# Kernel optimization log

Measured on AMD Instinct MI355X. Metric: run time of the kernel, lower is better.

The kernel has to match this reference:

```python
import jax, jax.numpy as jnp
import numpy as np

EPS = 1e-5

def rmsnorm(x, w):
    var = jnp.mean(x * x, axis=-1, keepdims=True)
    return x * jax.lax.rsqrt(var + EPS) * w


def setup_inputs() -> dict:
    key = jax.random.key(0)
    B, L, dim = 4, 2048, 1024
    d_inner, d_state, d_conv, dt_rank = 2 * dim, 16, 4, dim // 16
    ks = jax.random.split(key, 8)
    g = lambda k, shape, scale: (jax.random.normal(k, shape, jnp.float32) * scale)
    return {
        "x": g(ks[0], (B, L, dim), 1.0),
        "rms_w": jnp.ones((dim,), jnp.float32),
        "in_proj": g(ks[1], (dim, 2 * d_inner), dim ** -0.5),
        "conv_w": g(ks[2], (d_inner, d_conv), 0.25),
        "conv_b": jnp.zeros((d_inner,), jnp.float32),
        "x_proj": g(ks[3], (d_inner, dt_rank + 2 * d_state), d_inner ** -0.5),
        "dt_w": g(ks[4], (dt_rank, d_inner), dt_rank ** -0.5),
        # inverse-softplus(0.01): softplus(dt_b) ~ 0.01 at init, standard Mamba dt init
        "dt_b": jnp.full((d_inner,), float(np.log(np.expm1(0.01))), jnp.float32),
        # S4D-real init: A_n = -(n+1)
        "A_log": jnp.log(jnp.broadcast_to(jnp.arange(1, d_state + 1, dtype=jnp.float32), (d_inner, d_state))).copy(),
        "D": jnp.ones((d_inner,), jnp.float32),
        "out_proj": g(ks[5], (d_inner, dim), d_inner ** -0.5),
    }


def _mamba_block(x, rms_w, in_proj, conv_w, conv_b, x_proj, dt_w, dt_b, A_log, D, out_proj):
    B, L, dim = x.shape
    d_inner, K = conv_w.shape
    d_state = A_log.shape[1]
    dt_rank = dt_w.shape[0]

    xn = rmsnorm(x, rms_w)
    xz = xn @ in_proj                      # [B,L,2*d_inner]
    xi, z = jnp.split(xz, 2, axis=-1)

    # causal depthwise conv1d over L
    xc = jax.lax.conv_general_dilated(
        xi.transpose(0, 2, 1),             # [B,C,L]
        conv_w[:, None, :],                # [C,1,K]
        window_strides=(1,), padding=[(K - 1, 0)],
        feature_group_count=d_inner,
    ).transpose(0, 2, 1) + conv_b
    xi = jax.nn.silu(xc)                   # [B,L,d_inner]

    dbc = xi @ x_proj                      # [B,L,dt_rank+2*d_state]
    dt, Bm, Cm = jnp.split(dbc, [dt_rank, dt_rank + d_state], axis=-1)
    delta = jax.nn.softplus(dt @ dt_w + dt_b)  # [B,L,d_inner]
    A = -jnp.exp(A_log)                    # [d_inner,d_state]

    def step(h, inputs):
        d_t, x_t, B_t, C_t = inputs        # [B,d_inner],[B,d_inner],[B,d_state],[B,d_state]
        dA = jnp.exp(d_t[..., None] * A)   # [B,d_inner,d_state]
        h = dA * h + (d_t * x_t)[..., None] * B_t[:, None, :]
        y = jnp.einsum('bds,bs->bd', h, C_t)
        return h, y

    h0 = jnp.zeros((B, d_inner, d_state), x.dtype)
    xs = (delta.transpose(1, 0, 2), xi.transpose(1, 0, 2),
          Bm.transpose(1, 0, 2), Cm.transpose(1, 0, 2))
    _, ys = jax.lax.scan(step, h0, xs)     # ys: [L,B,d_inner]

    y = ys.transpose(1, 0, 2) + xi * D     # D skip connection
    y = y * jax.nn.silu(z)                 # output gate
    return x + y @ out_proj                # residual


def reference(x, rms_w, in_proj, conv_w, conv_b, x_proj, dt_w, dt_b, A_log, D, out_proj):
    return _mamba_block(x, rms_w, in_proj, conv_w, conv_b, x_proj, dt_w, dt_b, A_log, D, out_proj)
```

## Files before the change

kernel.cpp:

```cpp
#include <hip/hip_runtime.h>
#include <hip/hip_bf16.h>
#include <math.h>


#define ROWS 8192
#define DIM 1024
#define DINNER 2048
#define DSTATE 16
#define DTRANK 64
#define LSEQ 2048
#define NCHUNK 32
#define LCHUNK 64

#define LOG2E 1.4426950408889634f

typedef unsigned short ushort;
typedef __attribute__((ext_vector_type(8))) short short8;
typedef __attribute__((ext_vector_type(4))) float float4v;

__device__ inline ushort f2bf(float f) {
    __hip_bfloat16 h = __float2bfloat16(f);
    return *reinterpret_cast<ushort*>(&h);
}
__device__ inline float bf2f(ushort u) {
    union { unsigned int i; float f; } w; w.i = ((unsigned int)u) << 16; return w.f;
}

__device__ inline float fexp2(float x) {
#if __has_builtin(__builtin_amdgcn_exp2f)
    return __builtin_amdgcn_exp2f(x);
#else
    return __expf(x * 0.69314718056f);
#endif
}

__device__ inline void dma16(const void* g, void* l) {
    __builtin_amdgcn_global_load_lds(
        (const __attribute__((address_space(1))) unsigned int*)g,
        (__attribute__((address_space(3))) unsigned int*)l, 16, 0, 0);
}

__global__ __launch_bounds__(256)
void prep_kernel(const float* __restrict__ in_proj, ushort* __restrict__ bt1,
                 const float* __restrict__ out_proj, ushort* __restrict__ bt2,
                 const float* __restrict__ x_proj, ushort* __restrict__ bt3,
                 const float* __restrict__ dt_w, ushort* __restrict__ bt4,
                 const float* __restrict__ x, const float* __restrict__ rms_w,
                 ushort* __restrict__ xn, float* __restrict__ dbc) {
    __shared__ float tld[32][33];
    __shared__ float red[4];
    int bid = blockIdx.x, tid = threadIdx.x;
    if (bid < 6464) {
        const float* in; ushort* outT; int R, C, bx, by;
        if (bid < 4096)      { in = in_proj;  outT = bt1; R = 1024; C = 4096; bx = bid & 127; by = bid >> 7; }
        else if (bid < 6144) { int t = bid - 4096; in = out_proj; outT = bt2; R = 2048; C = 1024; bx = t & 31; by = t >> 5; }
        else if (bid < 6336) { int t = bid - 6144; in = x_proj;  outT = bt3; R = 2048; C = 96;  bx = t % 3;  by = t / 3; }
        else                 { int t = bid - 6336; in = dt_w;    outT = bt4; R = 64;   C = 2048; bx = t & 63; by = t >> 6; }
        int tx = tid & 31, ty = tid >> 5;
#pragma unroll
        for (int k = 0; k < 4; ++k)
            tld[ty + k * 8][tx] = in[(long)(by * 32 + ty + k * 8) * C + bx * 32 + tx];
        __syncthreads();
#pragma unroll
        for (int k = 0; k < 4; ++k)
            outT[(long)(bx * 32 + ty + k * 8) * R + by * 32 + tx] = f2bf(tld[tx][ty + k * 8]);
    } else if (bid < 14656) {
        int row = bid - 6464;
        float4 xv = ((const float4*)(x + (long)row * DIM))[tid];
        float ss = xv.x * xv.x + xv.y * xv.y + xv.z * xv.z + xv.w * xv.w;
        for (int off = 32; off > 0; off >>= 1) ss += __shfl_down(ss, off);
        if ((tid & 63) == 0) red[tid >> 6] = ss;
        __syncthreads();
        float scale = rsqrtf((red[0] + red[1] + red[2] + red[3]) / DIM + 1e-5f);
        float4 wv = ((const float4*)rms_w)[tid];
        ushort4 ov;
        ov.x = f2bf(xv.x * scale * wv.x);
        ov.y = f2bf(xv.y * scale * wv.y);
        ov.z = f2bf(xv.z * scale * wv.z);
        ov.w = f2bf(xv.w * scale * wv.w);
        ((ushort4*)xn)[(long)row * 256 + tid] = ov;
    } else {
        int idx = (bid - 14656) * 256 + tid;
        float4 z = {0.f, 0.f, 0.f, 0.f};
        ((float4*)dbc)[idx] = z;
    }
}

template <int MW, int NW, int MF, int NF, int EPI>
__global__ __launch_bounds__(MW * NW * 64, 2)
void gemm_ring(const ushort* __restrict__ A, int lda,
               const ushort* __restrict__ Bt, int ldbt,
               void* __restrict__ Cv, int ldc, int K,
               const float* __restrict__ aux) {
    constexpr int W    = MW * NW;
    constexpr int BLKM = MW * MF * 16;
    constexpr int BLKN = NW * NF * 16;
    constexpr int TILE = (BLKM + BLKN) * 32;
    __shared__ __align__(16) ushort lds[4 * TILE];

    const int tid  = threadIdx.x;
    const int w    = tid >> 6, lane = tid & 63;
    const int wm   = w / NW,   wn   = w % NW;
    const int quad = lane >> 4, l16 = lane & 15;
    const long row0 = (long)blockIdx.y * BLKM;
    const long col0 = (long)blockIdx.x * BLKN;

    const ushort* gA0 = A  + (row0 + (w    ) * 16 + l16) * lda  + quad * 8;
    const ushort* gA1 = A  + (row0 + (w + W) * 16 + l16) * lda  + quad * 8;
    const ushort* gB0 = Bt + (col0 + (w    ) * 16 + l16) * ldbt + quad * 8;
    const ushort* gB1 = Bt + (col0 + (w + W) * 16 + l16) * ldbt + quad * 8;

    const int NT = K >> 5;
    float4v acc[MF][NF] = {};

#define STAGE(kt) do {                                            \
        ushort* lb_ = lds + ((kt) & 3) * TILE;                    \
        const int ko_ = (kt) << 5;                                \
        dma16(gA0 + ko_, lb_ + (w    ) * 512);                    \
        dma16(gA1 + ko_, lb_ + (w + W) * 512);                    \
        dma16(gB0 + ko_, lb_ + BLKM * 32 + (w    ) * 512);        \
        dma16(gB1 + ko_, lb_ + BLKM * 32 + (w + W) * 512);        \
    } while (0)

    STAGE(0); STAGE(1); STAGE(2);
    asm volatile("s_waitcnt vmcnt(8)" ::: "memory");
    __builtin_amdgcn_s_barrier();
    __builtin_amdgcn_sched_barrier(0);

    for (int t = 0; t < NT; ++t) {
        const ushort* lb = lds + (t & 3) * TILE;
        short8 af[MF], bf[NF];
#pragma unroll
        for (int m = 0; m < MF; ++m)
            af[m] = *reinterpret_cast<const short8*>(
                &lb[(wm * MF + m) * 512 + lane * 8]);
#pragma unroll
        for (int n = 0; n < NF; ++n)
            bf[n] = *reinterpret_cast<const short8*>(
                &lb[BLKM * 32 + (wn * NF + n) * 512 + lane * 8]);
        if (t + 3 < NT) STAGE(t + 3);
        __builtin_amdgcn_s_setprio(1);
#pragma unroll
        for (int m = 0; m < MF; ++m)
#pragma unroll
            for (int n = 0; n < NF; ++n)
                acc[m][n] = __builtin_amdgcn_mfma_f32_16x16x32_bf16(
                    af[m], bf[n], acc[m][n], 0, 0, 0);
        __builtin_amdgcn_s_setprio(0);
        if (t < NT - 3)       asm volatile("s_waitcnt vmcnt(8)" ::: "memory");
        else if (t == NT - 3) asm volatile("s_waitcnt vmcnt(4)" ::: "memory");
        else if (t == NT - 2) asm volatile("s_waitcnt vmcnt(0)" ::: "memory");
        if (t < NT - 1) {
            __builtin_amdgcn_s_barrier();
            __builtin_amdgcn_sched_barrier(0);
        }
    }
#undef STAGE

#pragma unroll
    for (int m = 0; m < MF; ++m) {
#pragma unroll
        for (int n = 0; n < NF; ++n) {
            long rbase = row0 + wm * (MF * 16) + m * 16 + quad * 4;
            long c = col0 + wn * (NF * 16) + n * 16 + l16;
#pragma unroll
            for (int r = 0; r < 4; ++r) {
                float v = acc[m][n][r];
                long idx = (rbase + r) * (long)ldc + c;
                if (EPI == 2) ((float*)Cv)[idx] = v + aux[idx];
                else          ((ushort*)Cv)[idx] = f2bf(v);
            }
        }
    }
}

__global__ __launch_bounds__(256)
void xproj_conv_gemm(const ushort* __restrict__ xz,
                     const float* __restrict__ cw, const float* __restrict__ cb,
                     const ushort* __restrict__ bt3,
                     float* __restrict__ dbc) {
    __shared__ __align__(16) ushort As[128][32];
    __shared__ __align__(16) ushort Bs[128][32];
    int tid = threadIdx.x;
    int wave = tid >> 6, lane = tid & 63;
    int wm = wave >> 1, wn = wave & 1;
    int quad = lane >> 4, l16 = lane & 15;
    int row0 = blockIdx.y * 128;
    int ks0 = blockIdx.x * 512;
    int srow = tid >> 2, sseg = tid & 3;

    int r0 = (wave * 2 + 0) * 16 + (lane >> 2);
    int r1 = (wave * 2 + 1) * 16 + (lane >> 2);
    int ksl = (lane & 3) * 8;
    const ushort* b0 = bt3 + (long)r0 * 2048 + ks0 + ksl;
    const ushort* b1 = bt3 + (long)r1 * 2048 + ks0 + ksl;
    ushort* lB0 = &Bs[(wave * 2 + 0) * 16][0];
    ushort* lB1 = &Bs[(wave * 2 + 1) * 16][0];

    float4v acc[4][4] = {};

    for (int k0 = 0; k0 < 512; k0 += 32) {
        dma16(b0 + k0, lB0);
        dma16(b1 + k0, lB1);
#pragma unroll
        for (int it = 0; it < 2; ++it) {
            int r = srow + it * 64;
            long row = row0 + r;
            int l = (int)(row & (LSEQ - 1));
            int cch = ks0 + k0 + sseg * 8;
            short8 v[4];
#pragma unroll
            for (int t = 0; t < 4; ++t) {
                if (l - 3 + t >= 0) v[t] = *(const short8*)&xz[(row - 3 + t) * 4096 + cch];
                else { short8 zz = {0,0,0,0,0,0,0,0}; v[t] = zz; }
            }
            ushort o[8];
#pragma unroll
            for (int j = 0; j < 8; ++j) {
                float4 w = ((const float4*)cw)[cch + j];
                float a = cb[cch + j]
                        + bf2f((ushort)v[0][j]) * w.x + bf2f((ushort)v[1][j]) * w.y
                        + bf2f((ushort)v[2][j]) * w.z + bf2f((ushort)v[3][j]) * w.w;
                a = a / (1.f + __expf(-a));
                o[j] = f2bf(a);
            }
            *(short8*)&As[r][sseg * 8] = *(const short8*)o;
        }
        __syncthreads();

        short8 afrag[4], bfrag[4];
#pragma unroll
        for (int i = 0; i < 4; ++i)
            afrag[i] = *reinterpret_cast<const short8*>(&As[wm * 64 + i * 16 + l16][quad * 8]);
#pragma unroll
        for (int j = 0; j < 4; ++j)
            bfrag[j] = *reinterpret_cast<const short8*>(&Bs[wn * 64 + j * 16 + l16][quad * 8]);
#pragma unroll
        for (int i = 0; i < 4; ++i)
#pragma unroll
            for (int j = 0; j < 4; ++j)
                acc[i][j] = __builtin_amdgcn_mfma_f32_16x16x32_bf16(
                    afrag[i], bfrag[j], acc[i][j], 0, 0, 0);
        __syncthreads();
    }
#pragma unroll
    for (int i = 0; i < 4; ++i) {
#pragma unroll
        for (int j = 0; j < 4; ++j) {
            int rbase = row0 + wm * 64 + i * 16 + quad * 4;
            int c = wn * 64 + j * 16 + l16;
            if (c < 96) {
#pragma unroll
                for (int r = 0; r < 4; ++r)
                    atomicAdd(&dbc[(long)(rbase + r) * 96 + c], acc[i][j][r]);
            }
        }
    }
}

__global__ __launch_bounds__(256)
void mfma_gemm_dt(const float* __restrict__ A, int lda,
                  const ushort* __restrict__ Bt, int ldbt,
                  ushort* __restrict__ C, int ldc, int K,
                  const float* __restrict__ aux) {
    __shared__ __align__(16) ushort As[128][40];
    __shared__ __align__(16) ushort Bs[128][40];
    int tid = threadIdx.x;
    int wave = tid >> 6, lane = tid & 63;
    int wm = wave >> 1, wn = wave & 1;
    int quad = lane >> 4, l16 = lane & 15;
    int row0 = blockIdx.y * 128, col0 = blockIdx.x * 128;
    int srow = tid >> 2, sseg = tid & 3;

    float4v acc[4][4] = {};

    for (int k0 = 0; k0 < K; k0 += 32) {
#pragma unroll
        for (int it = 0; it < 2; ++it) {
            int r = srow + it * 64;
            const float* ap = A + (long)(row0 + r) * lda + k0 + sseg * 8;
            ushort tmp[8];
#pragma unroll
            for (int j = 0; j < 8; ++j) tmp[j] = f2bf(ap[j]);
            *reinterpret_cast<short8*>(&As[r][sseg * 8]) =
                *reinterpret_cast<const short8*>(tmp);
            const ushort* bp = Bt + (long)(col0 + r) * ldbt + k0 + sseg * 8;
            *reinterpret_cast<short8*>(&Bs[r][sseg * 8]) =
                *reinterpret_cast<const short8*>(bp);
        }
        __syncthreads();
        short8 afrag[4], bfrag[4];
#pragma unroll
        for (int i = 0; i < 4; ++i)
            afrag[i] = *reinterpret_cast<const short8*>(&As[wm * 64 + i * 16 + l16][quad * 8]);
#pragma unroll
        for (int j = 0; j < 4; ++j)
            bfrag[j] = *reinterpret_cast<const short8*>(&Bs[wn * 64 + j * 16 + l16][quad * 8]);
#pragma unroll
        for (int i = 0; i < 4; ++i)
#pragma unroll
            for (int j = 0; j < 4; ++j)
                acc[i][j] = __builtin_amdgcn_mfma_f32_16x16x32_bf16(
                    afrag[i], bfrag[j], acc[i][j], 0, 0, 0);
        __syncthreads();
    }
#pragma unroll
    for (int i = 0; i < 4; ++i) {
#pragma unroll
        for (int j = 0; j < 4; ++j) {
            int rbase = row0 + wm * 64 + i * 16 + quad * 4;
            int c = col0 + wn * 64 + j * 16 + l16;
#pragma unroll
            for (int r = 0; r < 4; ++r) {
                float v = acc[i][j][r] + aux[c];
                v = (v > 20.f) ? v : __logf(1.f + __expf(v));
                C[(long)(rbase + r) * ldc + c] = f2bf(v);
            }
        }
    }
}

__global__ __launch_bounds__(256)
void scan_part1(const ushort* __restrict__ xz,
                const ushort* __restrict__ dlt,
                const float* __restrict__ dbc,
                const float* __restrict__ A_log,
                const float* __restrict__ cw, const float* __restrict__ cb,
                float* __restrict__ hbuf,
                float* __restrict__ sdbuf) {
    int c = blockIdx.y * 256 + threadIdx.x;
    int b = blockIdx.z, g = blockIdx.x;
    float A2[16];
#pragma unroll
    for (int s = 0; s < 16; ++s) A2[s] = -__expf(A_log[c * 16 + s]) * LOG2E;
    float4 w = ((const float4*)cw)[c];
    float cbc = cb[c];
    float h[16] = {};
    float sumd = 0.f;
    long row0 = (long)b * LSEQ + (long)g * LCHUNK;
    int l0 = g * LCHUNK;
    float x0 = (l0 >= 3) ? bf2f(xz[(row0 - 3) * 4096 + c]) : 0.f;
    float x1 = (l0 >= 2) ? bf2f(xz[(row0 - 2) * 4096 + c]) : 0.f;
    float x2 = (l0 >= 1) ? bf2f(xz[(row0 - 1) * 4096 + c]) : 0.f;
    long row = row0;
    for (int l = 0; l < LCHUNK; ++l, ++row) {
        float x3 = bf2f(xz[row * 4096 + c]);
        float xc = cbc + x0 * w.x + x1 * w.y + x2 * w.z + x3 * w.w;
        xc = xc / (1.f + __expf(-xc));
        x0 = x1; x1 = x2; x2 = x3;
        float d = bf2f(dlt[row * 2048 + c]);
        const float* __restrict__ bc = dbc + row * 96;
        sumd += d;
        float dx = d * xc;
#pragma unroll
        for (int s = 0; s < 16; ++s)
            h[s] = fexp2(d * A2[s]) * h[s] + dx * bc[64 + s];
    }
    long hb = ((long)(b * NCHUNK + g) * 16) * 2048 + c;
#pragma unroll
    for (int s = 0; s < 16; ++s) hbuf[hb + (long)s * 2048] = h[s];
    sdbuf[(long)(b * NCHUNK + g) * 2048 + c] = sumd;
}

__global__ __launch_bounds__(256)
void scan_part2(float* __restrict__ hbuf, const float* __restrict__ sdbuf,
                const float* __restrict__ A_log) {
    int gl = blockIdx.x * 256 + threadIdx.x;
    int c = gl & 2047, s = (gl >> 11) & 15, b = gl >> 15;
    float A2 = -__expf(A_log[c * 16 + s]) * LOG2E;
    float hrun = 0.f;
    for (int g = 0; g < NCHUNK; ++g) {
        long hi = ((long)(b * NCHUNK + g) * 16 + s) * 2048 + c;
        float hout = hbuf[hi];
        float sd = sdbuf[(long)(b * NCHUNK + g) * 2048 + c];
        hbuf[hi] = hrun;
        hrun = fexp2(A2 * sd) * hrun + hout;
    }
}

__global__ __launch_bounds__(256)
void scan_part3(const ushort* __restrict__ xz,
                ushort* __restrict__ dlt,
                const float* __restrict__ dbc,
                const float* __restrict__ A_log,
                const float* __restrict__ cw, const float* __restrict__ cb,
                const float* __restrict__ Dp,
                const float* __restrict__ hbuf) {
    int c = blockIdx.y * 256 + threadIdx.x;
    int b = blockIdx.z, g = blockIdx.x;
    float A2[16], h[16];
#pragma unroll
    for (int s = 0; s < 16; ++s) A2[s] = -__expf(A_log[c * 16 + s]) * LOG2E;
    long hb = ((long)(b * NCHUNK + g) * 16) * 2048 + c;
#pragma unroll
    for (int s = 0; s < 16; ++s) h[s] = hbuf[hb + (long)s * 2048];
    float4 w = ((const float4*)cw)[c];
    float cbc = cb[c];
    float Dc = Dp[c];
    long row0 = (long)b * LSEQ + (long)g * LCHUNK;
    int l0 = g * LCHUNK;
    float x0 = (l0 >= 3) ? bf2f(xz[(row0 - 3) * 4096 + c]) : 0.f;
    float x1 = (l0 >= 2) ? bf2f(xz[(row0 - 2) * 4096 + c]) : 0.f;
    float x2 = (l0 >= 1) ? bf2f(xz[(row0 - 1) * 4096 + c]) : 0.f;
    long row = row0;
    for (int l = 0; l < LCHUNK; ++l, ++row) {
        float x3 = bf2f(xz[row * 4096 + c]);
        float xc = cbc + x0 * w.x + x1 * w.y + x2 * w.z + x3 * w.w;
        xc = xc / (1.f + __expf(-xc));
        x0 = x1; x1 = x2; x2 = x3;
        float d = bf2f(dlt[row * 2048 + c]);
        float z = bf2f(xz[row * 4096 + 2048 + c]);
        const float* __restrict__ bc = dbc + row * 96;
        float dx = d * xc;
        float y = 0.f;
#pragma unroll
        for (int s = 0; s < 16; ++s) {
            h[s] = fexp2(d * A2[s]) * h[s] + dx * bc[64 + s];
            y += h[s] * bc[80 + s];
        }
        float yv = (y + xc * Dc) * (z / (1.f + __expf(-z)));
        dlt[row * 2048 + c] = f2bf(yv);
    }
}

extern "C" void kernel_launch(void* const* d_in, const int* in_sizes, int n_in,
                              void* d_out, int out_size, void* d_ws, size_t ws_size,
                              hipStream_t stream) {
    const float* x        = (const float*)d_in[0];
    const float* rms_w    = (const float*)d_in[1];
    const float* in_proj  = (const float*)d_in[2];
    const float* conv_w   = (const float*)d_in[3];
    const float* conv_b   = (const float*)d_in[4];
    const float* x_proj   = (const float*)d_in[5];
    const float* dt_w     = (const float*)d_in[6];
    const float* dt_b     = (const float*)d_in[7];
    const float* A_log    = (const float*)d_in[8];
    const float* Dp       = (const float*)d_in[9];
    const float* out_proj = (const float*)d_in[10];
    float* out = (float*)d_out;

    char* p = (char*)d_ws;
    ushort* xz  = (ushort*)p;   p += (size_t)ROWS * 4096 * 2;
    ushort* dlt = (ushort*)p;   p += (size_t)ROWS * 2048 * 2;
    float*  dbc = (float*)p;    p += (size_t)ROWS * 96 * 4;
    ushort* bt1 = (ushort*)p;   p += (size_t)4096 * 1024 * 2;
    ushort* bt2 = (ushort*)p;   p += (size_t)1024 * 2048 * 2;
    ushort* bt3 = (ushort*)p;   p += (size_t)128 * 2048 * 2;
    ushort* bt4 = (ushort*)p;   p += (size_t)2048 * 64 * 2;
    ushort* xn  = (ushort*)p;   p += (size_t)ROWS * 1024 * 2;
    float* sdbuf = (float*)p;   p += (size_t)4 * NCHUNK * 2048 * 4;
    float* hbuf  = (float*)xn;

    prep_kernel<<<15424, 256, 0, stream>>>(in_proj, bt1, out_proj, bt2,
                                           x_proj, bt3, dt_w, bt4,
                                           x, rms_w, xn, dbc);
    gemm_ring<2, 4, 8, 4, 0><<<dim3(4096 / 256, ROWS / 256), 512, 0, stream>>>(
        xn, DIM, bt1, 1024, xz, 4096, DIM, nullptr);
    xproj_conv_gemm<<<dim3(4, ROWS / 128), 256, 0, stream>>>(
        xz, conv_w, conv_b, bt3, dbc);
    mfma_gemm_dt<<<dim3(2048 / 128, ROWS / 128), 256, 0, stream>>>(
        dbc, 96, bt4, 64, dlt, 2048, DTRANK, dt_b);
    scan_part1<<<dim3(NCHUNK, DINNER / 256, 4), 256, 0, stream>>>(
        xz, dlt, dbc, A_log, conv_w, conv_b, hbuf, sdbuf);
    scan_part2<<<512, 256, 0, stream>>>(hbuf, sdbuf, A_log);
    scan_part3<<<dim3(NCHUNK, DINNER / 256, 4), 256, 0, stream>>>(
        xz, dlt, dbc, A_log, conv_w, conv_b, Dp, hbuf);
    gemm_ring<2, 2, 4, 4, 2><<<dim3(DIM / 128, ROWS / 128), 256, 0, stream>>>(
        dlt, DINNER, bt2, DINNER, out, DIM, DINNER, x);
}
```

Measured before the change: 481.9 us.

## Split GEMM k-step into sub-phases interleaving DMA and MFMA; enlarge out_proj tile

```diff
diff --git a/kernel.cpp b/kernel.cpp
--- a/kernel.cpp
+++ b/kernel.cpp
@@ -38,6 +38,15 @@
     __builtin_amdgcn_global_load_lds(
         (const __attribute__((address_space(1))) unsigned int*)g,
         (__attribute__((address_space(3))) unsigned int*)l, 16, 0, 0);
+}
+
+template <int N> __device__ inline void vwait() {
+    if constexpr (N == 0)      asm volatile("s_waitcnt vmcnt(0)" ::: "memory");
+    else if constexpr (N == 3) asm volatile("s_waitcnt vmcnt(3)" ::: "memory");
+    else if constexpr (N == 4) asm volatile("s_waitcnt vmcnt(4)" ::: "memory");
+    else if constexpr (N == 6) asm volatile("s_waitcnt vmcnt(6)" ::: "memory");
+    else if constexpr (N == 8) asm volatile("s_waitcnt vmcnt(8)" ::: "memory");
+    else static_assert(N < 0, "unsupported vmcnt literal");
 }
 
 __global__ __launch_bounds__(256)
@@ -86,7 +95,7 @@
     }
 }
 
-template <int MW, int NW, int MF, int NF, int EPI>
+template <int MW, int NW, int MF, int NF, int SUBP, int EPI>
 __global__ __launch_bounds__(MW * NW * 64, 2)
 void gemm_ring(const ushort* __restrict__ A, int lda,
                const ushort* __restrict__ Bt, int ldbt,
@@ -96,6 +105,10 @@
     constexpr int BLKM = MW * MF * 16;
     constexpr int BLKN = NW * NF * 16;
     constexpr int TILE = (BLKM + BLKN) * 32;
+    constexpr int NA   = BLKM / (16 * W);
+    constexpr int NB   = BLKN / (16 * W);
+    constexpr int DPT  = NA + NB;
+    constexpr int MH   = MF / SUBP;
     __shared__ __align__(16) ushort lds[4 * TILE];
 
     const int tid  = threadIdx.x;
@@ -105,57 +118,94 @@
     const long row0 = (long)blockIdx.y * BLKM;
     const long col0 = (long)blockIdx.x * BLKN;
 
-    const ushort* gA0 = A  + (row0 + (w    ) * 16 + l16) * lda  + quad * 8;
-    const ushort* gA1 = A  + (row0 + (w + W) * 16 + l16) * lda  + quad * 8;
-    const ushort* gB0 = Bt + (col0 + (w    ) * 16 + l16) * ldbt + quad * 8;
-    const ushort* gB1 = Bt + (col0 + (w + W) * 16 + l16) * ldbt + quad * 8;
+    const ushort* gA[NA];
+    const ushort* gB[NB];
+#pragma unroll
+    for (int i = 0; i < NA; ++i)
+        gA[i] = A + (row0 + (w + i * W) * 16 + l16) * lda + quad * 8;
+#pragma unroll
+    for (int i = 0; i < NB; ++i)
+        gB[i] = Bt + (col0 + (w + i * W) * 16 + l16) * ldbt + quad * 8;
 
     const int NT = K >> 5;
     float4v acc[MF][NF] = {};
 
-#define STAGE(kt) do {                                            \
-        ushort* lb_ = lds + ((kt) & 3) * TILE;                    \
-        const int ko_ = (kt) << 5;                                \
-        dma16(gA0 + ko_, lb_ + (w    ) * 512);                    \
-        dma16(gA1 + ko_, lb_ + (w + W) * 512);                    \
-        dma16(gB0 + ko_, lb_ + BLKM * 32 + (w    ) * 512);        \
-        dma16(gB1 + ko_, lb_ + BLKM * 32 + (w + W) * 512);        \
-    } while (0)
-
-    STAGE(0); STAGE(1); STAGE(2);
-    asm volatile("s_waitcnt vmcnt(8)" ::: "memory");
+    auto stageA = [&](int kt) {
+        ushort* lb = lds + (kt & 3) * TILE;
+        const int ko = kt << 5;
+#pragma unroll
+        for (int i = 0; i < NA; ++i)
+            dma16(gA[i] + ko, lb + (w + i * W) * 512);
+    };
+    auto stageB = [&](int kt) {
+        ushort* lb = lds + (kt & 3) * TILE + BLKM * 32;
+        const int ko = kt << 5;
+#pragma unroll
+        for (int i = 0; i < NB; ++i)
+            dma16(gB[i] + ko, lb + (w + i * W) * 512);
+    };
+    auto tailwait = [&](int t) {
+        if (t + 3 < NT)      vwait<2 * DPT>();
+        else if (t + 2 < NT) vwait<DPT>();
+        else                 vwait<0>();
+    };
+
+    stageA(0); stageB(0); stageA(1); stageB(1); stageA(2); stageB(2);
+    vwait<2 * DPT>();
     __builtin_amdgcn_s_barrier();
-    __builtin_amdgcn_sched_barrier(0);
 
     for (int t = 0; t < NT; ++t) {
-        const ushort* lb = lds + (t & 3) * TILE;
-        short8 af[MF], bf[NF];
-#pragma unroll
-        for (int m = 0; m < MF; ++m)
+        const ushort* lb  = lds + (t & 3) * TILE;
+        const ushort* lbB = lb + BLKM * 32;
+        const bool stg = (t + 3 < NT);
+        short8 af[MF], bfr[NF];
+
+#pragma unroll
+        for (int n = 0; n < NF; ++n)
+            bfr[n] = *reinterpret_cast<const short8*>(
+                &lbB[(wn * NF + n) * 512 + lane * 8]);
+#pragma unroll
+        for (int m = 0; m < MH; ++m)
             af[m] = *reinterpret_cast<const short8*>(
                 &lb[(wm * MF + m) * 512 + lane * 8]);
-#pragma unroll
-        for (int n = 0; n < NF; ++n)
-            bf[n] = *reinterpret_cast<const short8*>(
-                &lb[BLKM * 32 + (wn * NF + n) * 512 + lane * 8]);
-        if (t + 3 < NT) STAGE(t + 3);
+        if (stg) { stageA(t + 3); if (SUBP == 1) stageB(t + 3); }
+        __builtin_amdgcn_s_barrier();
+        asm volatile("s_waitcnt lgkmcnt(0)" ::: "memory");
+        __builtin_amdgcn_sched_barrier(0);
         __builtin_amdgcn_s_setprio(1);
 #pragma unroll
-        for (int m = 0; m < MF; ++m)
+        for (int m = 0; m < MH; ++m)
 #pragma unroll
             for (int n = 0; n < NF; ++n)
                 acc[m][n] = __builtin_amdgcn_mfma_f32_16x16x32_bf16(
-                    af[m], bf[n], acc[m][n], 0, 0, 0);
+                    af[m], bfr[n], acc[m][n], 0, 0, 0);
         __builtin_amdgcn_s_setprio(0);
-        if (t < NT - 3)       asm volatile("s_waitcnt vmcnt(8)" ::: "memory");
-        else if (t == NT - 3) asm volatile("s_waitcnt vmcnt(4)" ::: "memory");
-        else if (t == NT - 2) asm volatile("s_waitcnt vmcnt(0)" ::: "memory");
-        if (t < NT - 1) {
+
+        if (SUBP == 1) {
+            tailwait(t);
+            if (t < NT - 1) __builtin_amdgcn_s_barrier();
+        } else {
             __builtin_amdgcn_s_barrier();
+#pragma unroll
+            for (int m = MH; m < MF; ++m)
+                af[m] = *reinterpret_cast<const short8*>(
+                    &lb[(wm * MF + m) * 512 + lane * 8]);
+            if (stg) stageB(t + 3);
+            __builtin_amdgcn_s_barrier();
+            asm volatile("s_waitcnt lgkmcnt(0)" ::: "memory");
             __builtin_amdgcn_sched_barrier(0);
-        }
-    }
-#undef STAGE
+            __builtin_amdgcn_s_setprio(1);
+#pragma unroll
+            for (int m = MH; m < MF; ++m)
+#pragma unroll
+                for (int n = 0; n < NF; ++n)
+                    acc[m][n] = __builtin_amdgcn_mfma_f32_16x16x32_bf16(
+                        af[m], bfr[n], acc[m][n], 0, 0, 0);
+            __builtin_amdgcn_s_setprio(0);
+            tailwait(t);
+            if (t < NT - 1) __builtin_amdgcn_s_barrier();
+        }
+    }
 
 #pragma unroll
     for (int m = 0; m < MF; ++m) {
@@ -454,7 +504,7 @@
     prep_kernel<<<15424, 256, 0, stream>>>(in_proj, bt1, out_proj, bt2,
                                            x_proj, bt3, dt_w, bt4,
                                            x, rms_w, xn, dbc);
-    gemm_ring<2, 4, 8, 4, 0><<<dim3(4096 / 256, ROWS / 256), 512, 0, stream>>>(
+    gemm_ring<2, 4, 8, 4, 2, 0><<<dim3(4096 / 256, ROWS / 256), 512, 0, stream>>>(
         xn, DIM, bt1, 1024, xz, 4096, DIM, nullptr);
     xproj_conv_gemm<<<dim3(4, ROWS / 128), 256, 0, stream>>>(
         xz, conv_w, conv_b, bt3, dbc);
@@ -465,6 +515,6 @@
     scan_part2<<<512, 256, 0, stream>>>(hbuf, sdbuf, A_log);
     scan_part3<<<dim3(NCHUNK, DINNER / 256, 4), 256, 0, stream>>>(
         xz, dlt, dbc, A_log, conv_w, conv_b, Dp, hbuf);
-    gemm_ring<2, 2, 4, 4, 2><<<dim3(DIM / 128, ROWS / 128), 256, 0, stream>>>(
+    gemm_ring<4, 2, 4, 4, 1, 2><<<dim3(DIM / 128, ROWS / 256), 512, 0, stream>>>(
         dlt, DINNER, bt2, DINNER, out, DIM, DINNER, x);
 }
```

Measured after the change: 479.2 us. Within noise of the previous version (-0.6%).
